# Optimization experiments

Hardware: AMD Instinct MI355X
Metric: run time of the kernel (lower is better)

Reference implementation:

```python
import jax, jax.numpy as jnp
import numpy as np

N_NODES = 500000
N_EDGES = 16000000
NDIM = 2
HID = 8


def setup_inputs() -> dict:
    key = jax.random.key(0)
    ks = jax.random.split(key, 12)
    x = jax.random.normal(ks[0], (N_NODES, NDIM), dtype=jnp.float32)
    edge_index = jax.random.randint(ks[1], (2, N_EDGES), 0, N_NODES, dtype=jnp.int64)
    def lin(k, fan_in, fan_out):
        s = 1.0 / np.sqrt(fan_in)
        return jax.random.uniform(k, (fan_in, fan_out), jnp.float32, -s, s)
    return {
        "x": x,
        "edge_index": edge_index,
        "W1": lin(ks[2], NDIM, HID), "b1": jnp.zeros((HID,), jnp.float32),
        "W2": lin(ks[3], HID, HID), "b2": jnp.zeros((HID,), jnp.float32),
        "W3": lin(ks[4], HID, HID), "b3": jnp.zeros((HID,), jnp.float32),
        "Wr1": lin(ks[5], HID, HID), "br1": jnp.zeros((HID,), jnp.float32),
        "Wr2": lin(ks[6], HID, 1), "br2": jnp.zeros((1,), jnp.float32),
    }


def reference(x, edge_index, W1, b1, W2, b2, W3, b3, Wr1, br1, Wr2, br2):
    N = x.shape[0]
    loop = jnp.arange(N, dtype=edge_index.dtype)
    src = jnp.concatenate([edge_index[0], loop])  # [E+N] message sources j
    dst = jnp.concatenate([edge_index[1], loop])  # [E+N] message targets i
    # GCN symmetric normalization with self-loops: D^{-1/2} (A+I) D^{-1/2}
    deg = jax.ops.segment_sum(jnp.ones(src.shape[0], x.dtype), dst, num_segments=N)
    dinv = jnp.where(deg > 0, jax.lax.rsqrt(jnp.maximum(deg, 1.0)), 0.0)
    norm = (dinv[src] * dinv[dst])[:, None]  # [E+N, 1]

    def gcn_conv(h, W, b):
        h = h @ W  # transform first (small hidden dim)
        agg = jax.ops.segment_sum(h[src] * norm, dst, num_segments=N)
        return agg + b

    h = jax.nn.elu(gcn_conv(x, W1, b1))   # dropout inactive (eval mode)
    h = jax.nn.elu(gcn_conv(h, W2, b2))
    h = jax.nn.elu(gcn_conv(h, W3, b3))
    pooled = jnp.mean(h, axis=0, keepdims=True)  # global_mean_pool, single graph -> [1, HID]
    value = jax.nn.elu(pooled @ Wr1 + br1) @ Wr2 + br2  # [1, 1]
    return value
```

## Files before the change

### kernel.cpp

```cpp
#include <hip/hip_runtime.h>
#include <hip/hip_fp16.h>

#define NNODES 500000
#define HID 8
#define BIN_SHIFT 9
#define BINW 512
#define NBIN 977
#define SCAN_BLK 1024
#define SGRID 256
#define CAP 28
#define BATCH 4096
#define BUFCAP 18432
#define AGRID 512
#define ABLK 256

typedef int intx4 __attribute__((ext_vector_type(4)));

__device__ __forceinline__ unsigned int packh2(float a, float b) {
    __half2 h = __floats2half2_rn(a, b);
    return *reinterpret_cast<unsigned int*>(&h);
}
__device__ __forceinline__ float2 unpackh2(unsigned int u) {
    __half2 h = *reinterpret_cast<__half2*>(&u);
    return __half22float2(h);
}
__device__ __forceinline__ float elu(float t) { return t > 0.0f ? t : expm1f(t); }
__device__ __forceinline__ int nt_load_i(const int* p) { return __builtin_nontemporal_load(p); }
__device__ __forceinline__ intx4 nt_load_i4(const intx4* p) { return __builtin_nontemporal_load(p); }

__device__ __forceinline__ unsigned int enc_e4m3(float x) {
    unsigned sgn = (__float_as_uint(x) >> 31) << 7;
    float ax = fabsf(x);
    if (ax >= 448.f) return sgn | 0x7E;
    if (ax < 0.015625f) {
        unsigned q = (unsigned)__float2int_rn(ax * 512.0f);
        return sgn | q;
    }
    unsigned u = __float_as_uint(ax);
    int te = (int)((u >> 23) & 0xFF) - 120;
    unsigned m = u & 0x7FFFFF;
    unsigned r = (m + 0x7FFFF + ((m >> 20) & 1)) >> 20;
    unsigned code = ((unsigned)te << 3) + r;
    if (code > 0x7E) code = 0x7E;
    return sgn | code;
}

__device__ __forceinline__ float2 dec2_e4m3(unsigned int b01) {
    unsigned int x = (b01 & 0xFFu) | ((b01 & 0xFF00u) << 8);
    unsigned int h = ((x & 0x00800080u) << 8) | ((x & 0x007F007Fu) << 7);
    __half2 hv = *reinterpret_cast<__half2*>(&h);
    const __half2 s256 = __floats2half2_rn(256.0f, 256.0f);
    hv = __hmul2(hv, s256);
    return __half22float2(hv);
}

__global__ void binhist_kernel(const int* __restrict__ dst, int E, int* __restrict__ gbinhist) {
    __shared__ int hist[NBIN];
    for (int b = threadIdx.x; b < NBIN; b += blockDim.x) hist[b] = 0;
    __syncthreads();
    int stride = gridDim.x * blockDim.x;
    const intx4* d4 = (const intx4*)dst;
    int n4 = E >> 2;
    for (int e = blockIdx.x * blockDim.x + threadIdx.x; e < n4; e += stride) {
        intx4 d = nt_load_i4(&d4[e]);
        atomicAdd(&hist[d.x >> BIN_SHIFT], 1);
        atomicAdd(&hist[d.y >> BIN_SHIFT], 1);
        atomicAdd(&hist[d.z >> BIN_SHIFT], 1);
        atomicAdd(&hist[d.w >> BIN_SHIFT], 1);
    }
    int tail0 = n4 << 2;
    for (int e = tail0 + blockIdx.x * blockDim.x + threadIdx.x; e < E; e += stride)
        atomicAdd(&hist[dst[e] >> BIN_SHIFT], 1);
    __syncthreads();
    for (int b = threadIdx.x; b < NBIN; b += blockDim.x) {
        int c = hist[b];
        if (c) atomicAdd(&gbinhist[b], c);
    }
}

__global__ void scan1_kernel(const int* __restrict__ deg, int* __restrict__ excl,
                             int* __restrict__ bsum, int N) {
    __shared__ int sm[SCAN_BLK];
    int tid = threadIdx.x;
    int gid = blockIdx.x * SCAN_BLK + tid;
    int v = (gid < N) ? deg[gid] : 0;
    int x = v;
    sm[tid] = x;
    __syncthreads();
    for (int off = 1; off < SCAN_BLK; off <<= 1) {
        int t = (tid >= off) ? sm[tid - off] : 0;
        __syncthreads();
        x += t;
        sm[tid] = x;
        __syncthreads();
    }
    if (gid < N) excl[gid] = x - v;
    if (tid == SCAN_BLK - 1) bsum[blockIdx.x] = x;
}

__global__ void scan2_kernel(int* __restrict__ bsum, int nb) {
    __shared__ int sm[SCAN_BLK];
    int tid = threadIdx.x;
    int v = (tid < nb) ? bsum[tid] : 0;
    int x = v;
    sm[tid] = x;
    __syncthreads();
    for (int off = 1; off < SCAN_BLK; off <<= 1) {
        int t = (tid >= off) ? sm[tid - off] : 0;
        __syncthreads();
        x += t;
        sm[tid] = x;
        __syncthreads();
    }
    if (tid < nb) bsum[tid] = x - v;
}

__global__ void scan3b_kernel(const int* __restrict__ binexcl, const int* __restrict__ bsum,
                              int* __restrict__ ptr_bins, int* __restrict__ gcursor, int E) {
    int i = blockIdx.x * blockDim.x + threadIdx.x;
    if (i < NBIN) {
        int p = binexcl[i] + bsum[i / SCAN_BLK];
        ptr_bins[i] = p;
        gcursor[i] = p;
    }
    if (i == 0) ptr_bins[NBIN] = E;
}

__global__ void __launch_bounds__(1024) binscatter_kernel(
        const int* __restrict__ src, const int* __restrict__ dst,
        int E, int* __restrict__ gcursor, int* __restrict__ packed) {
    __shared__ int cnt[NBIN];
    __shared__ int bucket[NBIN][CAP];
    __shared__ int fq_bin[NBIN];
    __shared__ int fq_pos[NBIN];
    __shared__ int fq_n;
    int tid = threadIdx.x;
    int slice = (((E + SGRID - 1) / SGRID) + 3) & ~3;
    int e0 = blockIdx.x * slice;
    int e1 = min(E, e0 + slice);
    if (e0 >= e1) return;
    for (int b = tid; b < NBIN; b += 1024) cnt[b] = 0;
    if (tid == 0) fq_n = 0;
    __syncthreads();
    for (int base = e0; base < e1; base += BATCH) {
        int bend = min(e1, base + BATCH);
        int k = base + tid * 4;
        if (k + 4 <= bend) {
            intx4 d = nt_load_i4((const intx4*)(dst + k));
            intx4 s = nt_load_i4((const intx4*)(src + k));
#pragma unroll
            for (int j = 0; j < 4; ++j) {
                int dd = (j == 0) ? d.x : (j == 1) ? d.y : (j == 2) ? d.z : d.w;
                int ss = (j == 0) ? s.x : (j == 1) ? s.y : (j == 2) ? s.z : s.w;
                int b = dd >> BIN_SHIFT;
                int val = (ss << BIN_SHIFT) | (dd & (BINW - 1));
                int slot = atomicAdd(&cnt[b], 1);
                if (slot < CAP) bucket[b][slot] = val;
                else { int gp = atomicAdd(&gcursor[b], 1); packed[gp] = val; }
            }
        } else {
            for (int kk = k; kk < bend; ++kk) {
                int dd = nt_load_i(&dst[kk]);
                int ss = nt_load_i(&src[kk]);
                int b = dd >> BIN_SHIFT;
                int val = (ss << BIN_SHIFT) | (dd & (BINW - 1));
                int slot = atomicAdd(&cnt[b], 1);
                if (slot < CAP) bucket[b][slot] = val;
                else { int gp = atomicAdd(&gcursor[b], 1); packed[gp] = val; }
            }
        }
        __syncthreads();
        if (tid < NBIN) {
            int c = min(cnt[tid], CAP);
            if (c >= 16) {
                int idx = atomicAdd(&fq_n, 1);
                fq_bin[idx] = tid;
                fq_pos[idx] = atomicAdd(&gcursor[tid], 16);
            }
        }
        __syncthreads();
        int nf = fq_n;
        for (int w = tid; w < nf * 16; w += 1024) {
            int q = w >> 4, j = w & 15;
            packed[fq_pos[q] + j] = bucket[fq_bin[q]][j];
        }
        __syncthreads();
        if (tid < NBIN) {
            int c = min(cnt[tid], CAP);
            if (c >= 16) {
                int rem = c - 16;
                for (int j = 0; j < rem; ++j) bucket[tid][j] = bucket[tid][16 + j];
                cnt[tid] = rem;
            } else {
                cnt[tid] = c;
            }
        }
        if (tid == 0) fq_n = 0;
        __syncthreads();
    }
    if (tid < NBIN) {
        int c = min(cnt[tid], CAP);
        if (c > 0) {
            int pos = atomicAdd(&gcursor[tid], c);
            for (int j = 0; j < c; ++j) packed[pos + j] = bucket[tid][j];
        }
    }
}

__global__ void __launch_bounds__(512) binsort_kernel(
        const int* __restrict__ ptr_bins, int* __restrict__ ssrc,
        int* __restrict__ ptr, const float* __restrict__ x,
        unsigned int* __restrict__ t1, int N, int E) {
    __shared__ int buf[BUFCAP];
    __shared__ int hist[BINW];
    __shared__ int scn[BINW];
    __shared__ int cursor[BINW];
    int bin = blockIdx.x;
    int tid = threadIdx.x;
    int base = ptr_bins[bin];
    int len = min(ptr_bins[bin + 1] - base, BUFCAP);
    int node_base = bin << BIN_SHIFT;
    int nn = min(BINW, N - node_base);
    hist[tid] = 0;
    __syncthreads();
    for (int k = tid; k < len; k += 512) {
        int v = nt_load_i(&ssrc[base + k]);
        buf[k] = v;
        atomicAdd(&hist[v & (BINW - 1)], 1);
    }
    __syncthreads();
    int orig = hist[tid];
    int x_ = orig;
    scn[tid] = x_;
    __syncthreads();
    for (int off = 1; off < BINW; off <<= 1) {
        int t = (tid >= off) ? scn[tid - off] : 0;
        __syncthreads();
        x_ += t;
        scn[tid] = x_;
        __syncthreads();
    }
    if (tid < nn) {
        int ex = x_ - orig;
        int node = node_base + tid;
        ptr[node] = base + ex;
        cursor[tid] = ex;
        float dv = rsqrtf((float)orig + 1.0f);
        float2 xv = *reinterpret_cast<const float2*>(x + 2 * (size_t)node);
        t1[node] = packh2(dv * xv.x, dv * xv.y);
    }
    if (bin == NBIN - 1 && tid == 0) ptr[N] = E;
    __syncthreads();
    for (int k = tid; k < len; k += 512) {
        int v = buf[k];
        int pos = atomicAdd(&cursor[v & (BINW - 1)], 1);
        ssrc[base + pos] = v >> BIN_SHIFT;
    }
}

__global__ void __launch_bounds__(ABLK) agg1_kernel(
        const unsigned int* __restrict__ t1, const int* __restrict__ ptr,
        const int* __restrict__ ssrc, const float* __restrict__ W1,
        const float* __restrict__ b1, const float* __restrict__ W2,
        uint2* __restrict__ t2, int N) {
    int stride = AGRID * ABLK;
    for (int i = blockIdx.x * ABLK + threadIdx.x; i < N; i += stride) {
        float2 s = unpackh2(t1[i]);
        int e0 = ptr[i], e1 = ptr[i + 1];
#pragma unroll 8
        for (int k = e0; k < e1; ++k) {
            float2 p = unpackh2(t1[nt_load_i(&ssrc[k])]);
            s.x += p.x; s.y += p.y;
        }
        float dv = rsqrtf((float)(e1 - e0) + 1.0f);
        float h[HID];
#pragma unroll
        for (int c = 0; c < HID; ++c)
            h[c] = elu(dv * (s.x * W1[c] + s.y * W1[HID + c]) + b1[c]);
        float g[HID];
#pragma unroll
        for (int c = 0; c < HID; ++c) {
            float acc = 0.0f;
#pragma unroll
            for (int k = 0; k < HID; ++k) acc += h[k] * W2[k * HID + c];
            g[c] = dv * acc;
        }
        unsigned int lo = enc_e4m3(g[0]) | (enc_e4m3(g[1]) << 8) |
                          (enc_e4m3(g[2]) << 16) | (enc_e4m3(g[3]) << 24);
        unsigned int hi = enc_e4m3(g[4]) | (enc_e4m3(g[5]) << 8) |
                          (enc_e4m3(g[6]) << 16) | (enc_e4m3(g[7]) << 24);
        __builtin_nontemporal_store(lo, &t2[i].x);
        __builtin_nontemporal_store(hi, &t2[i].y);
    }
}

__global__ void __launch_bounds__(ABLK) agg2_kernel(
        const uint2* __restrict__ tab, const int* __restrict__ ptr,
        const int* __restrict__ ssrc, const float* __restrict__ b2,
        const float* __restrict__ W3, uint2* __restrict__ t3, int N) {
    int stride = AGRID * ABLK;
    for (int i = blockIdx.x * ABLK + threadIdx.x; i < N; i += stride) {
        uint2 u = tab[i];
        float2 p0 = dec2_e4m3(u.x), p1 = dec2_e4m3(u.x >> 16);
        float2 p2 = dec2_e4m3(u.y), p3 = dec2_e4m3(u.y >> 16);
        float s0 = p0.x, s1 = p0.y, s2 = p1.x, s3 = p1.y;
        float s4 = p2.x, s5 = p2.y, s6 = p3.x, s7 = p3.y;
        int e0 = ptr[i], e1 = ptr[i + 1];
#pragma unroll 8
        for (int k = e0; k < e1; ++k) {
            uint2 w = tab[nt_load_i(&ssrc[k])];
            float2 q0 = dec2_e4m3(w.x), q1 = dec2_e4m3(w.x >> 16);
            float2 q2 = dec2_e4m3(w.y), q3 = dec2_e4m3(w.y >> 16);
            s0 += q0.x; s1 += q0.y; s2 += q1.x; s3 += q1.y;
            s4 += q2.x; s5 += q2.y; s6 += q3.x; s7 += q3.y;
        }
        float dv = rsqrtf((float)(e1 - e0) + 1.0f);
        float h[HID] = {elu(dv * s0 + b2[0]), elu(dv * s1 + b2[1]),
                        elu(dv * s2 + b2[2]), elu(dv * s3 + b2[3]),
                        elu(dv * s4 + b2[4]), elu(dv * s5 + b2[5]),
                        elu(dv * s6 + b2[6]), elu(dv * s7 + b2[7])};
        float g[HID];
#pragma unroll
        for (int c = 0; c < HID; ++c) {
            float acc = 0.0f;
#pragma unroll
            for (int k = 0; k < HID; ++k) acc += h[k] * W3[k * HID + c];
            g[c] = dv * acc;
        }
        unsigned int lo = enc_e4m3(g[0]) | (enc_e4m3(g[1]) << 8) |
                          (enc_e4m3(g[2]) << 16) | (enc_e4m3(g[3]) << 24);
        unsigned int hi = enc_e4m3(g[4]) | (enc_e4m3(g[5]) << 8) |
                          (enc_e4m3(g[6]) << 16) | (enc_e4m3(g[7]) << 24);
        __builtin_nontemporal_store(lo, &t3[i].x);
        __builtin_nontemporal_store(hi, &t3[i].y);
    }
}

__global__ void __launch_bounds__(ABLK) agg3_kernel(
        const uint2* __restrict__ tab, const int* __restrict__ ptr,
        const int* __restrict__ ssrc, const float* __restrict__ b3,
        double* __restrict__ pooled, int N) {
    float v[HID];
#pragma unroll
    for (int c = 0; c < HID; ++c) v[c] = 0.0f;
    int stride = AGRID * ABLK;
    for (int i = blockIdx.x * ABLK + threadIdx.x; i < N; i += stride) {
        uint2 u = tab[i];
        float2 p0 = dec2_e4m3(u.x), p1 = dec2_e4m3(u.x >> 16);
        float2 p2 = dec2_e4m3(u.y), p3 = dec2_e4m3(u.y >> 16);
        float s0 = p0.x, s1 = p0.y, s2 = p1.x, s3 = p1.y;
        float s4 = p2.x, s5 = p2.y, s6 = p3.x, s7 = p3.y;
        int e0 = ptr[i], e1 = ptr[i + 1];
#pragma unroll 8
        for (int k = e0; k < e1; ++k) {
            uint2 w = tab[nt_load_i(&ssrc[k])];
            float2 q0 = dec2_e4m3(w.x), q1 = dec2_e4m3(w.x >> 16);
            float2 q2 = dec2_e4m3(w.y), q3 = dec2_e4m3(w.y >> 16);
            s0 += q0.x; s1 += q0.y; s2 += q1.x; s3 += q1.y;
            s4 += q2.x; s5 += q2.y; s6 += q3.x; s7 += q3.y;
        }
        float dv = rsqrtf((float)(e1 - e0) + 1.0f);
        v[0] += elu(dv * s0 + b3[0]); v[1] += elu(dv * s1 + b3[1]);
        v[2] += elu(dv * s2 + b3[2]); v[3] += elu(dv * s3 + b3[3]);
        v[4] += elu(dv * s4 + b3[4]); v[5] += elu(dv * s5 + b3[5]);
        v[6] += elu(dv * s6 + b3[6]); v[7] += elu(dv * s7 + b3[7]);
    }
#pragma unroll
    for (int c = 0; c < HID; ++c) {
        float s = v[c];
        for (int off = 32; off > 0; off >>= 1) s += __shfl_down(s, off);
        v[c] = s;
    }
    __shared__ float sm[4][HID];
    int lane = threadIdx.x & 63;
    int wv = threadIdx.x >> 6;
    if (lane == 0) {
#pragma unroll
        for (int c = 0; c < HID; ++c) sm[wv][c] = v[c];
    }
    __syncthreads();
    if (threadIdx.x == 0) {
#pragma unroll
        for (int c = 0; c < HID; ++c) {
            float s = sm[0][c] + sm[1][c] + sm[2][c] + sm[3][c];
            atomicAdd(&pooled[c], (double)s);
        }
    }
}

__global__ void head_kernel(const double* __restrict__ pooled, const float* __restrict__ Wr1,
                            const float* __restrict__ br1, const float* __restrict__ Wr2,
                            const float* __restrict__ br2, float* __restrict__ out, int N) {
    if (threadIdx.x != 0 || blockIdx.x != 0) return;
    float p[HID];
#pragma unroll
    for (int k = 0; k < HID; ++k) p[k] = (float)(pooled[k] / (double)N);
    float hdn[HID];
#pragma unroll
    for (int j = 0; j < HID; ++j) {
        float s = br1[j];
#pragma unroll
        for (int k = 0; k < HID; ++k) s += p[k] * Wr1[k * HID + j];
        hdn[j] = elu(s);
    }
    float v = br2[0];
#pragma unroll
    for (int j = 0; j < HID; ++j) v += hdn[j] * Wr2[j];
    out[0] = v;
}

extern "C" void kernel_launch(void* const* d_in, const int* in_sizes, int n_in,
                              void* d_out, int out_size, void* d_ws, size_t ws_size,
                              hipStream_t stream) {
    const float* x   = (const float*)d_in[0];
    const int*   ei  = (const int*)d_in[1];
    const float* W1  = (const float*)d_in[2];
    const float* b1  = (const float*)d_in[3];
    const float* W2  = (const float*)d_in[4];
    const float* b2  = (const float*)d_in[5];
    const float* W3  = (const float*)d_in[6];
    const float* b3  = (const float*)d_in[7];
    const float* Wr1 = (const float*)d_in[8];
    const float* br1 = (const float*)d_in[9];
    const float* Wr2 = (const float*)d_in[10];
    const float* br2 = (const float*)d_in[11];
    float* out = (float*)d_out;

    const int N = NNODES;
    const int E = in_sizes[1] / 2;
    const int* srcp = ei;
    const int* dstp = ei + E;

    double* pooled    = (double*)d_ws;
    unsigned int* t1  = (unsigned int*)(pooled + HID);
    uint2* t2         = (uint2*)(t1 + N);
    uint2* t3         = t2 + N;
    int* gbinhist     = (int*)(t3 + N);
    int* binexcl      = gbinhist + NBIN;
    int* bsum         = binexcl + NBIN;
    int* ptr_bins     = bsum + 1024;
    int* gcursor      = ptr_bins + NBIN + 1;
    int* ptr          = gcursor + NBIN;
    int* ssrc         = ptr + N + 1;

    hipMemsetAsync(gbinhist, 0, NBIN * sizeof(int), stream);
    hipMemsetAsync(pooled, 0, HID * sizeof(double), stream);

    const int BLK = 256;

    binhist_kernel<<<128, 1024, 0, stream>>>(dstp, E, gbinhist);
    scan1_kernel<<<1, SCAN_BLK, 0, stream>>>(gbinhist, binexcl, bsum, NBIN);
    scan2_kernel<<<1, SCAN_BLK, 0, stream>>>(bsum, 1);
    scan3b_kernel<<<(NBIN + BLK - 1) / BLK, BLK, 0, stream>>>(binexcl, bsum, ptr_bins, gcursor, E);
    binscatter_kernel<<<SGRID, 1024, 0, stream>>>(srcp, dstp, E, gcursor, ssrc);
    binsort_kernel<<<NBIN, 512, 0, stream>>>(ptr_bins, ssrc, ptr, x, t1, N, E);

    agg1_kernel<<<AGRID, ABLK, 0, stream>>>(t1, ptr, ssrc, W1, b1, W2, t2, N);
    agg2_kernel<<<AGRID, ABLK, 0, stream>>>(t2, ptr, ssrc, b2, W3, t3, N);
    agg3_kernel<<<AGRID, ABLK, 0, stream>>>(t3, ptr, ssrc, b3, pooled, N);

    head_kernel<<<1, 64, 0, stream>>>(pooled, Wr1, br1, Wr2, br2, out, N);
}
```

Before: 712.7 us.

## Use edge-balanced per-block aggregation with LDS-staged indices and shared atomics

Each of the three aggregation kernels now handles a 256-node tile per block. The block stages the tile's CSR pointers and up to 9216 source indices into LDS, then splits the tile's edges evenly across threads. A thread finds its first node by binary search and flushes its partial sums into shared-memory accumulators with atomics whenever it crosses a node boundary. This targets load imbalance from per-node degree variance (avg degree ~32) and gives coalesced index loads. In exchange it adds LDS atomics, extra barriers, and fewer gather loads in flight per thread, since each thread walks about 128 edges serially without unrolling.

```diff
diff --git a/kernel.cpp b/kernel.cpp
--- a/kernel.cpp
+++ b/kernel.cpp
@@ -11,8 +11,8 @@
 #define CAP 28
 #define BATCH 4096
 #define BUFCAP 18432
-#define AGRID 512
-#define ABLK 256
+#define ABIN 256
+#define EBUF 9216
 
 typedef int intx4 __attribute__((ext_vector_type(4)));
 
@@ -258,25 +258,56 @@
     }
 }
 
-__global__ void __launch_bounds__(ABLK) agg1_kernel(
+
+__global__ void __launch_bounds__(256) agg1_kernel(
         const unsigned int* __restrict__ t1, const int* __restrict__ ptr,
         const int* __restrict__ ssrc, const float* __restrict__ W1,
         const float* __restrict__ b1, const float* __restrict__ W2,
         uint2* __restrict__ t2, int N) {
-    int stride = AGRID * ABLK;
-    for (int i = blockIdx.x * ABLK + threadIdx.x; i < N; i += stride) {
-        float2 s = unpackh2(t1[i]);
-        int e0 = ptr[i], e1 = ptr[i + 1];
-#pragma unroll 8
-        for (int k = e0; k < e1; ++k) {
-            float2 p = unpackh2(t1[nt_load_i(&ssrc[k])]);
-            s.x += p.x; s.y += p.y;
-        }
-        float dv = rsqrtf((float)(e1 - e0) + 1.0f);
+    __shared__ int lbuf[EBUF];
+    __shared__ int lptr[ABIN + 1];
+    __shared__ float accum[ABIN][2];
+    int tid = threadIdx.x;
+    int n0 = blockIdx.x * ABIN;
+    int nn = min(ABIN, N - n0);
+    for (int j = tid; j <= nn; j += 256) lptr[j] = ptr[n0 + j];
+    if (tid < nn) { accum[tid][0] = 0.f; accum[tid][1] = 0.f; }
+    __syncthreads();
+    int E0 = lptr[0];
+    int len = lptr[nn] - E0;
+    for (int k = tid; k < min(len, EBUF); k += 256) lbuf[k] = nt_load_i(&ssrc[E0 + k]);
+    __syncthreads();
+    int C = (len + ABIN - 1) >> 8;
+    int kb = tid * C, ke = min(len, kb + C);
+    if (kb < ke) {
+        int lo = 0, hi = nn - 1, target = E0 + kb;
+        while (lo < hi) { int mid = (lo + hi + 1) >> 1; if (lptr[mid] <= target) lo = mid; else hi = mid - 1; }
+        int node = lo;
+        float sx = 0.f, sy = 0.f;
+        for (int k = kb; k < ke; ++k) {
+            int eg = E0 + k;
+            if (eg >= lptr[node + 1]) {
+                atomicAdd(&accum[node][0], sx); atomicAdd(&accum[node][1], sy);
+                sx = 0.f; sy = 0.f;
+                do { node++; } while (eg >= lptr[node + 1]);
+            }
+            int sidx = (k < EBUF) ? lbuf[k] : nt_load_i(&ssrc[E0 + k]);
+            float2 p = unpackh2(t1[sidx]);
+            sx += p.x; sy += p.y;
+        }
+        atomicAdd(&accum[node][0], sx); atomicAdd(&accum[node][1], sy);
+    }
+    __syncthreads();
+    if (tid < nn) {
+        int i = n0 + tid;
+        int deg = lptr[tid + 1] - lptr[tid];
+        float dv = rsqrtf((float)deg + 1.0f);
+        float2 sl = unpackh2(t1[i]);
+        float sx = accum[tid][0] + sl.x, sy = accum[tid][1] + sl.y;
         float h[HID];
 #pragma unroll
         for (int c = 0; c < HID; ++c)
-            h[c] = elu(dv * (s.x * W1[c] + s.y * W1[HID + c]) + b1[c]);
+            h[c] = elu(dv * (sx * W1[c] + sy * W1[HID + c]) + b1[c]);
         float g[HID];
 #pragma unroll
         for (int c = 0; c < HID; ++c) {
@@ -294,31 +325,72 @@
     }
 }
 
-__global__ void __launch_bounds__(ABLK) agg2_kernel(
+__global__ void __launch_bounds__(256) agg2_kernel(
         const uint2* __restrict__ tab, const int* __restrict__ ptr,
         const int* __restrict__ ssrc, const float* __restrict__ b2,
         const float* __restrict__ W3, uint2* __restrict__ t3, int N) {
-    int stride = AGRID * ABLK;
-    for (int i = blockIdx.x * ABLK + threadIdx.x; i < N; i += stride) {
-        uint2 u = tab[i];
-        float2 p0 = dec2_e4m3(u.x), p1 = dec2_e4m3(u.x >> 16);
-        float2 p2 = dec2_e4m3(u.y), p3 = dec2_e4m3(u.y >> 16);
-        float s0 = p0.x, s1 = p0.y, s2 = p1.x, s3 = p1.y;
-        float s4 = p2.x, s5 = p2.y, s6 = p3.x, s7 = p3.y;
-        int e0 = ptr[i], e1 = ptr[i + 1];
-#pragma unroll 8
-        for (int k = e0; k < e1; ++k) {
-            uint2 w = tab[nt_load_i(&ssrc[k])];
+    __shared__ int lbuf[EBUF];
+    __shared__ int lptr[ABIN + 1];
+    __shared__ float accum[ABIN][HID];
+    int tid = threadIdx.x;
+    int n0 = blockIdx.x * ABIN;
+    int nn = min(ABIN, N - n0);
+    for (int j = tid; j <= nn; j += 256) lptr[j] = ptr[n0 + j];
+    if (tid < nn) {
+#pragma unroll
+        for (int c = 0; c < HID; ++c) accum[tid][c] = 0.f;
+    }
+    __syncthreads();
+    int E0 = lptr[0];
+    int len = lptr[nn] - E0;
+    for (int k = tid; k < min(len, EBUF); k += 256) lbuf[k] = nt_load_i(&ssrc[E0 + k]);
+    __syncthreads();
+    int C = (len + ABIN - 1) >> 8;
+    int kb = tid * C, ke = min(len, kb + C);
+    if (kb < ke) {
+        int lo = 0, hi = nn - 1, target = E0 + kb;
+        while (lo < hi) { int mid = (lo + hi + 1) >> 1; if (lptr[mid] <= target) lo = mid; else hi = mid - 1; }
+        int node = lo;
+        float s0 = 0.f, s1 = 0.f, s2 = 0.f, s3 = 0.f, s4 = 0.f, s5 = 0.f, s6 = 0.f, s7 = 0.f;
+        for (int k = kb; k < ke; ++k) {
+            int eg = E0 + k;
+            if (eg >= lptr[node + 1]) {
+                atomicAdd(&accum[node][0], s0); atomicAdd(&accum[node][1], s1);
+                atomicAdd(&accum[node][2], s2); atomicAdd(&accum[node][3], s3);
+                atomicAdd(&accum[node][4], s4); atomicAdd(&accum[node][5], s5);
+                atomicAdd(&accum[node][6], s6); atomicAdd(&accum[node][7], s7);
+                s0 = s1 = s2 = s3 = s4 = s5 = s6 = s7 = 0.f;
+                do { node++; } while (eg >= lptr[node + 1]);
+            }
+            int sidx = (k < EBUF) ? lbuf[k] : nt_load_i(&ssrc[E0 + k]);
+            uint2 w = tab[sidx];
             float2 q0 = dec2_e4m3(w.x), q1 = dec2_e4m3(w.x >> 16);
             float2 q2 = dec2_e4m3(w.y), q3 = dec2_e4m3(w.y >> 16);
             s0 += q0.x; s1 += q0.y; s2 += q1.x; s3 += q1.y;
             s4 += q2.x; s5 += q2.y; s6 += q3.x; s7 += q3.y;
         }
-        float dv = rsqrtf((float)(e1 - e0) + 1.0f);
-        float h[HID] = {elu(dv * s0 + b2[0]), elu(dv * s1 + b2[1]),
-                        elu(dv * s2 + b2[2]), elu(dv * s3 + b2[3]),
-                        elu(dv * s4 + b2[4]), elu(dv * s5 + b2[5]),
-                        elu(dv * s6 + b2[6]), elu(dv * s7 + b2[7])};
+        atomicAdd(&accum[node][0], s0); atomicAdd(&accum[node][1], s1);
+        atomicAdd(&accum[node][2], s2); atomicAdd(&accum[node][3], s3);
+        atomicAdd(&accum[node][4], s4); atomicAdd(&accum[node][5], s5);
+        atomicAdd(&accum[node][6], s6); atomicAdd(&accum[node][7], s7);
+    }
+    __syncthreads();
+    if (tid < nn) {
+        int i = n0 + tid;
+        int deg = lptr[tid + 1] - lptr[tid];
+        float dv = rsqrtf((float)deg + 1.0f);
+        uint2 u = tab[i];
+        float2 p0 = dec2_e4m3(u.x), p1 = dec2_e4m3(u.x >> 16);
+        float2 p2 = dec2_e4m3(u.y), p3 = dec2_e4m3(u.y >> 16);
+        float h[HID];
+        h[0] = elu(dv * (accum[tid][0] + p0.x) + b2[0]);
+        h[1] = elu(dv * (accum[tid][1] + p0.y) + b2[1]);
+        h[2] = elu(dv * (accum[tid][2] + p1.x) + b2[2]);
+        h[3] = elu(dv * (accum[tid][3] + p1.y) + b2[3]);
+        h[4] = elu(dv * (accum[tid][4] + p2.x) + b2[4]);
+        h[5] = elu(dv * (accum[tid][5] + p2.y) + b2[5]);
+        h[6] = elu(dv * (accum[tid][6] + p3.x) + b2[6]);
+        h[7] = elu(dv * (accum[tid][7] + p3.y) + b2[7]);
         float g[HID];
 #pragma unroll
         for (int c = 0; c < HID; ++c) {
@@ -336,34 +408,75 @@
     }
 }
 
-__global__ void __launch_bounds__(ABLK) agg3_kernel(
+__global__ void __launch_bounds__(256) agg3_kernel(
         const uint2* __restrict__ tab, const int* __restrict__ ptr,
         const int* __restrict__ ssrc, const float* __restrict__ b3,
         double* __restrict__ pooled, int N) {
-    float v[HID];
-#pragma unroll
-    for (int c = 0; c < HID; ++c) v[c] = 0.0f;
-    int stride = AGRID * ABLK;
-    for (int i = blockIdx.x * ABLK + threadIdx.x; i < N; i += stride) {
-        uint2 u = tab[i];
-        float2 p0 = dec2_e4m3(u.x), p1 = dec2_e4m3(u.x >> 16);
-        float2 p2 = dec2_e4m3(u.y), p3 = dec2_e4m3(u.y >> 16);
-        float s0 = p0.x, s1 = p0.y, s2 = p1.x, s3 = p1.y;
-        float s4 = p2.x, s5 = p2.y, s6 = p3.x, s7 = p3.y;
-        int e0 = ptr[i], e1 = ptr[i + 1];
-#pragma unroll 8
-        for (int k = e0; k < e1; ++k) {
-            uint2 w = tab[nt_load_i(&ssrc[k])];
+    __shared__ int lbuf[EBUF];
+    __shared__ int lptr[ABIN + 1];
+    __shared__ float accum[ABIN][HID];
+    __shared__ float sm[4][HID];
+    int tid = threadIdx.x;
+    int n0 = blockIdx.x * ABIN;
+    int nn = min(ABIN, N - n0);
+    for (int j = tid; j <= nn; j += 256) lptr[j] = ptr[n0 + j];
+    if (tid < nn) {
+#pragma unroll
+        for (int c = 0; c < HID; ++c) accum[tid][c] = 0.f;
+    }
+    __syncthreads();
+    int E0 = lptr[0];
+    int len = lptr[nn] - E0;
+    for (int k = tid; k < min(len, EBUF); k += 256) lbuf[k] = nt_load_i(&ssrc[E0 + k]);
+    __syncthreads();
+    int C = (len + ABIN - 1) >> 8;
+    int kb = tid * C, ke = min(len, kb + C);
+    if (kb < ke) {
+        int lo = 0, hi = nn - 1, target = E0 + kb;
+        while (lo < hi) { int mid = (lo + hi + 1) >> 1; if (lptr[mid] <= target) lo = mid; else hi = mid - 1; }
+        int node = lo;
+        float s0 = 0.f, s1 = 0.f, s2 = 0.f, s3 = 0.f, s4 = 0.f, s5 = 0.f, s6 = 0.f, s7 = 0.f;
+        for (int k = kb; k < ke; ++k) {
+            int eg = E0 + k;
+            if (eg >= lptr[node + 1]) {
+                atomicAdd(&accum[node][0], s0); atomicAdd(&accum[node][1], s1);
+                atomicAdd(&accum[node][2], s2); atomicAdd(&accum[node][3], s3);
+                atomicAdd(&accum[node][4], s4); atomicAdd(&accum[node][5], s5);
+                atomicAdd(&accum[node][6], s6); atomicAdd(&accum[node][7], s7);
+                s0 = s1 = s2 = s3 = s4 = s5 = s6 = s7 = 0.f;
+                do { node++; } while (eg >= lptr[node + 1]);
+            }
+            int sidx = (k < EBUF) ? lbuf[k] : nt_load_i(&ssrc[E0 + k]);
+            uint2 w = tab[sidx];
             float2 q0 = dec2_e4m3(w.x), q1 = dec2_e4m3(w.x >> 16);
             float2 q2 = dec2_e4m3(w.y), q3 = dec2_e4m3(w.y >> 16);
             s0 += q0.x; s1 += q0.y; s2 += q1.x; s3 += q1.y;
             s4 += q2.x; s5 += q2.y; s6 += q3.x; s7 += q3.y;
         }
-        float dv = rsqrtf((float)(e1 - e0) + 1.0f);
-        v[0] += elu(dv * s0 + b3[0]); v[1] += elu(dv * s1 + b3[1]);
-        v[2] += elu(dv * s2 + b3[2]); v[3] += elu(dv * s3 + b3[3]);
-        v[4] += elu(dv * s4 + b3[4]); v[5] += elu(dv * s5 + b3[5]);
-        v[6] += elu(dv * s6 + b3[6]); v[7] += elu(dv * s7 + b3[7]);
+        atomicAdd(&accum[node][0], s0); atomicAdd(&accum[node][1], s1);
+        atomicAdd(&accum[node][2], s2); atomicAdd(&accum[node][3], s3);
+        atomicAdd(&accum[node][4], s4); atomicAdd(&accum[node][5], s5);
+        atomicAdd(&accum[node][6], s6); atomicAdd(&accum[node][7], s7);
+    }
+    __syncthreads();
+    float v[HID];
+#pragma unroll
+    for (int c = 0; c < HID; ++c) v[c] = 0.f;
+    if (tid < nn) {
+        int i = n0 + tid;
+        int deg = lptr[tid + 1] - lptr[tid];
+        float dv = rsqrtf((float)deg + 1.0f);
+        uint2 u = tab[i];
+        float2 p0 = dec2_e4m3(u.x), p1 = dec2_e4m3(u.x >> 16);
+        float2 p2 = dec2_e4m3(u.y), p3 = dec2_e4m3(u.y >> 16);
+        v[0] = elu(dv * (accum[tid][0] + p0.x) + b3[0]);
+        v[1] = elu(dv * (accum[tid][1] + p0.y) + b3[1]);
+        v[2] = elu(dv * (accum[tid][2] + p1.x) + b3[2]);
+        v[3] = elu(dv * (accum[tid][3] + p1.y) + b3[3]);
+        v[4] = elu(dv * (accum[tid][4] + p2.x) + b3[4]);
+        v[5] = elu(dv * (accum[tid][5] + p2.y) + b3[5]);
+        v[6] = elu(dv * (accum[tid][6] + p3.x) + b3[6]);
+        v[7] = elu(dv * (accum[tid][7] + p3.y) + b3[7]);
     }
 #pragma unroll
     for (int c = 0; c < HID; ++c) {
@@ -371,7 +484,6 @@
         for (int off = 32; off > 0; off >>= 1) s += __shfl_down(s, off);
         v[c] = s;
     }
-    __shared__ float sm[4][HID];
     int lane = threadIdx.x & 63;
     int wv = threadIdx.x >> 6;
     if (lane == 0) {
@@ -447,6 +559,7 @@
     hipMemsetAsync(pooled, 0, HID * sizeof(double), stream);
 
     const int BLK = 256;
+    const int aggGrid = (N + ABIN - 1) / ABIN;
 
     binhist_kernel<<<128, 1024, 0, stream>>>(dstp, E, gbinhist);
     scan1_kernel<<<1, SCAN_BLK, 0, stream>>>(gbinhist, binexcl, bsum, NBIN);
@@ -455,9 +568,9 @@
     binscatter_kernel<<<SGRID, 1024, 0, stream>>>(srcp, dstp, E, gcursor, ssrc);
     binsort_kernel<<<NBIN, 512, 0, stream>>>(ptr_bins, ssrc, ptr, x, t1, N, E);
 
-    agg1_kernel<<<AGRID, ABLK, 0, stream>>>(t1, ptr, ssrc, W1, b1, W2, t2, N);
-    agg2_kernel<<<AGRID, ABLK, 0, stream>>>(t2, ptr, ssrc, b2, W3, t3, N);
-    agg3_kernel<<<AGRID, ABLK, 0, stream>>>(t3, ptr, ssrc, b3, pooled, N);
+    agg1_kernel<<<aggGrid, BLK, 0, stream>>>(t1, ptr, ssrc, W1, b1, W2, t2, N);
+    agg2_kernel<<<aggGrid, BLK, 0, stream>>>(t2, ptr, ssrc, b2, W3, t3, N);
+    agg3_kernel<<<aggGrid, BLK, 0, stream>>>(t3, ptr, ssrc, b3, pooled, N);
 
     head_kernel<<<1, 64, 0, stream>>>(pooled, Wr1, br1, Wr2, br2, out, N);
 }
```

Measured after the change: 772.3 us. 8.4% more time.

## Stage per-block CSR neighbor indices in LDS with coalesced loads

Applied to the files above, without the earlier changes.

The aggregation kernels switch from a grid-stride loop to one block per 256 destination nodes. Each block first loads its contiguous ssrc segment into shared memory with coalesced loads, using an XOR swizzle against bank conflicts. Threads then read neighbor indices from LDS instead of making strided per-thread global loads. Segments longer than the buffer fall back to global loads. The cost is about 37KB of LDS per block, which limits occupancy, plus two block barriers, and agg3 now issues one atomic per block across many more blocks (~1954).

```diff
diff --git a/kernel.cpp b/kernel.cpp
--- a/kernel.cpp
+++ b/kernel.cpp
@@ -11,8 +11,9 @@
 #define CAP 28
 #define BATCH 4096
 #define BUFCAP 18432
-#define AGRID 512
-#define ABLK 256
+#define ABIN 256
+#define EBUF 9216
+#define LIDX(k) ((k) ^ (((k) >> 5) & 31))
 
 typedef int intx4 __attribute__((ext_vector_type(4)));
 
@@ -258,112 +259,150 @@
     }
 }
 
-__global__ void __launch_bounds__(ABLK) agg1_kernel(
+__global__ void __launch_bounds__(256) agg1_kernel(
         const unsigned int* __restrict__ t1, const int* __restrict__ ptr,
         const int* __restrict__ ssrc, const float* __restrict__ W1,
         const float* __restrict__ b1, const float* __restrict__ W2,
         uint2* __restrict__ t2, int N) {
-    int stride = AGRID * ABLK;
-    for (int i = blockIdx.x * ABLK + threadIdx.x; i < N; i += stride) {
-        float2 s = unpackh2(t1[i]);
-        int e0 = ptr[i], e1 = ptr[i + 1];
+    __shared__ int lbuf[EBUF];
+    __shared__ int lptr[ABIN + 1];
+    int tid = threadIdx.x;
+    int n0 = blockIdx.x * ABIN;
+    int nn = min(ABIN, N - n0);
+    for (int j = tid; j <= nn; j += 256) lptr[j] = ptr[n0 + j];
+    __syncthreads();
+    int E0 = lptr[0];
+    int len = lptr[nn] - E0;
+    int lim = min(len, EBUF);
+    for (int k = tid; k < lim; k += 256) lbuf[LIDX(k)] = nt_load_i(&ssrc[E0 + k]);
+    __syncthreads();
+    if (tid >= nn) return;
+    int i = n0 + tid;
+    int kb = lptr[tid] - E0, ke = lptr[tid + 1] - E0;
+    float2 s = unpackh2(t1[i]);
 #pragma unroll 8
-        for (int k = e0; k < e1; ++k) {
-            float2 p = unpackh2(t1[nt_load_i(&ssrc[k])]);
-            s.x += p.x; s.y += p.y;
-        }
-        float dv = rsqrtf((float)(e1 - e0) + 1.0f);
-        float h[HID];
-#pragma unroll
-        for (int c = 0; c < HID; ++c)
-            h[c] = elu(dv * (s.x * W1[c] + s.y * W1[HID + c]) + b1[c]);
-        float g[HID];
-#pragma unroll
-        for (int c = 0; c < HID; ++c) {
-            float acc = 0.0f;
-#pragma unroll
-            for (int k = 0; k < HID; ++k) acc += h[k] * W2[k * HID + c];
-            g[c] = dv * acc;
-        }
-        unsigned int lo = enc_e4m3(g[0]) | (enc_e4m3(g[1]) << 8) |
-                          (enc_e4m3(g[2]) << 16) | (enc_e4m3(g[3]) << 24);
-        unsigned int hi = enc_e4m3(g[4]) | (enc_e4m3(g[5]) << 8) |
-                          (enc_e4m3(g[6]) << 16) | (enc_e4m3(g[7]) << 24);
-        __builtin_nontemporal_store(lo, &t2[i].x);
-        __builtin_nontemporal_store(hi, &t2[i].y);
-    }
-}
-
-__global__ void __launch_bounds__(ABLK) agg2_kernel(
+    for (int k = kb; k < ke; ++k) {
+        int sidx = (k < EBUF) ? lbuf[LIDX(k)] : nt_load_i(&ssrc[E0 + k]);
+        float2 p = unpackh2(t1[sidx]);
+        s.x += p.x; s.y += p.y;
+    }
+    float dv = rsqrtf((float)(ke - kb) + 1.0f);
+    float h[HID];
+#pragma unroll
+    for (int c = 0; c < HID; ++c)
+        h[c] = elu(dv * (s.x * W1[c] + s.y * W1[HID + c]) + b1[c]);
+    float g[HID];
+#pragma unroll
+    for (int c = 0; c < HID; ++c) {
+        float acc = 0.0f;
+#pragma unroll
+        for (int k = 0; k < HID; ++k) acc += h[k] * W2[k * HID + c];
+        g[c] = dv * acc;
+    }
+    unsigned int lo = enc_e4m3(g[0]) | (enc_e4m3(g[1]) << 8) |
+                      (enc_e4m3(g[2]) << 16) | (enc_e4m3(g[3]) << 24);
+    unsigned int hi = enc_e4m3(g[4]) | (enc_e4m3(g[5]) << 8) |
+                      (enc_e4m3(g[6]) << 16) | (enc_e4m3(g[7]) << 24);
+    __builtin_nontemporal_store(lo, &t2[i].x);
+    __builtin_nontemporal_store(hi, &t2[i].y);
+}
+
+__global__ void __launch_bounds__(256) agg2_kernel(
         const uint2* __restrict__ tab, const int* __restrict__ ptr,
         const int* __restrict__ ssrc, const float* __restrict__ b2,
         const float* __restrict__ W3, uint2* __restrict__ t3, int N) {
-    int stride = AGRID * ABLK;
-    for (int i = blockIdx.x * ABLK + threadIdx.x; i < N; i += stride) {
+    __shared__ int lbuf[EBUF];
+    __shared__ int lptr[ABIN + 1];
+    int tid = threadIdx.x;
+    int n0 = blockIdx.x * ABIN;
+    int nn = min(ABIN, N - n0);
+    for (int j = tid; j <= nn; j += 256) lptr[j] = ptr[n0 + j];
+    __syncthreads();
+    int E0 = lptr[0];
+    int len = lptr[nn] - E0;
+    int lim = min(len, EBUF);
+    for (int k = tid; k < lim; k += 256) lbuf[LIDX(k)] = nt_load_i(&ssrc[E0 + k]);
+    __syncthreads();
+    if (tid >= nn) return;
+    int i = n0 + tid;
+    int kb = lptr[tid] - E0, ke = lptr[tid + 1] - E0;
+    uint2 u = tab[i];
+    float2 p0 = dec2_e4m3(u.x), p1 = dec2_e4m3(u.x >> 16);
+    float2 p2 = dec2_e4m3(u.y), p3 = dec2_e4m3(u.y >> 16);
+    float s0 = p0.x, s1 = p0.y, s2 = p1.x, s3 = p1.y;
+    float s4 = p2.x, s5 = p2.y, s6 = p3.x, s7 = p3.y;
+#pragma unroll 8
+    for (int k = kb; k < ke; ++k) {
+        int sidx = (k < EBUF) ? lbuf[LIDX(k)] : nt_load_i(&ssrc[E0 + k]);
+        uint2 w = tab[sidx];
+        float2 q0 = dec2_e4m3(w.x), q1 = dec2_e4m3(w.x >> 16);
+        float2 q2 = dec2_e4m3(w.y), q3 = dec2_e4m3(w.y >> 16);
+        s0 += q0.x; s1 += q0.y; s2 += q1.x; s3 += q1.y;
+        s4 += q2.x; s5 += q2.y; s6 += q3.x; s7 += q3.y;
+    }
+    float dv = rsqrtf((float)(ke - kb) + 1.0f);
+    float h[HID] = {elu(dv * s0 + b2[0]), elu(dv * s1 + b2[1]),
+                    elu(dv * s2 + b2[2]), elu(dv * s3 + b2[3]),
+                    elu(dv * s4 + b2[4]), elu(dv * s5 + b2[5]),
+                    elu(dv * s6 + b2[6]), elu(dv * s7 + b2[7])};
+    float g[HID];
+#pragma unroll
+    for (int c = 0; c < HID; ++c) {
+        float acc = 0.0f;
+#pragma unroll
+        for (int k = 0; k < HID; ++k) acc += h[k] * W3[k * HID + c];
+        g[c] = dv * acc;
+    }
+    unsigned int lo = enc_e4m3(g[0]) | (enc_e4m3(g[1]) << 8) |
+                      (enc_e4m3(g[2]) << 16) | (enc_e4m3(g[3]) << 24);
+    unsigned int hi = enc_e4m3(g[4]) | (enc_e4m3(g[5]) << 8) |
+                      (enc_e4m3(g[6]) << 16) | (enc_e4m3(g[7]) << 24);
+    __builtin_nontemporal_store(lo, &t3[i].x);
+    __builtin_nontemporal_store(hi, &t3[i].y);
+}
+
+__global__ void __launch_bounds__(256) agg3_kernel(
+        const uint2* __restrict__ tab, const int* __restrict__ ptr,
+        const int* __restrict__ ssrc, const float* __restrict__ b3,
+        double* __restrict__ pooled, int N) {
+    __shared__ int lbuf[EBUF];
+    __shared__ int lptr[ABIN + 1];
+    __shared__ float sm[4][HID];
+    int tid = threadIdx.x;
+    int n0 = blockIdx.x * ABIN;
+    int nn = min(ABIN, N - n0);
+    for (int j = tid; j <= nn; j += 256) lptr[j] = ptr[n0 + j];
+    __syncthreads();
+    int E0 = lptr[0];
+    int len = lptr[nn] - E0;
+    int lim = min(len, EBUF);
+    for (int k = tid; k < lim; k += 256) lbuf[LIDX(k)] = nt_load_i(&ssrc[E0 + k]);
+    __syncthreads();
+    float v[HID];
+#pragma unroll
+    for (int c = 0; c < HID; ++c) v[c] = 0.f;
+    if (tid < nn) {
+        int i = n0 + tid;
+        int kb = lptr[tid] - E0, ke = lptr[tid + 1] - E0;
         uint2 u = tab[i];
         float2 p0 = dec2_e4m3(u.x), p1 = dec2_e4m3(u.x >> 16);
         float2 p2 = dec2_e4m3(u.y), p3 = dec2_e4m3(u.y >> 16);
         float s0 = p0.x, s1 = p0.y, s2 = p1.x, s3 = p1.y;
         float s4 = p2.x, s5 = p2.y, s6 = p3.x, s7 = p3.y;
-        int e0 = ptr[i], e1 = ptr[i + 1];
 #pragma unroll 8
-        for (int k = e0; k < e1; ++k) {
-            uint2 w = tab[nt_load_i(&ssrc[k])];
+        for (int k = kb; k < ke; ++k) {
+            int sidx = (k < EBUF) ? lbuf[LIDX(k)] : nt_load_i(&ssrc[E0 + k]);
+            uint2 w = tab[sidx];
             float2 q0 = dec2_e4m3(w.x), q1 = dec2_e4m3(w.x >> 16);
             float2 q2 = dec2_e4m3(w.y), q3 = dec2_e4m3(w.y >> 16);
             s0 += q0.x; s1 += q0.y; s2 += q1.x; s3 += q1.y;
             s4 += q2.x; s5 += q2.y; s6 += q3.x; s7 += q3.y;
         }
-        float dv = rsqrtf((float)(e1 - e0) + 1.0f);
-        float h[HID] = {elu(dv * s0 + b2[0]), elu(dv * s1 + b2[1]),
-                        elu(dv * s2 + b2[2]), elu(dv * s3 + b2[3]),
-                        elu(dv * s4 + b2[4]), elu(dv * s5 + b2[5]),
-                        elu(dv * s6 + b2[6]), elu(dv * s7 + b2[7])};
-        float g[HID];
-#pragma unroll
-        for (int c = 0; c < HID; ++c) {
-            float acc = 0.0f;
-#pragma unroll
-            for (int k = 0; k < HID; ++k) acc += h[k] * W3[k * HID + c];
-            g[c] = dv * acc;
-        }
-        unsigned int lo = enc_e4m3(g[0]) | (enc_e4m3(g[1]) << 8) |
-                          (enc_e4m3(g[2]) << 16) | (enc_e4m3(g[3]) << 24);
-        unsigned int hi = enc_e4m3(g[4]) | (enc_e4m3(g[5]) << 8) |
-                          (enc_e4m3(g[6]) << 16) | (enc_e4m3(g[7]) << 24);
-        __builtin_nontemporal_store(lo, &t3[i].x);
-        __builtin_nontemporal_store(hi, &t3[i].y);
-    }
-}
-
-__global__ void __launch_bounds__(ABLK) agg3_kernel(
-        const uint2* __restrict__ tab, const int* __restrict__ ptr,
-        const int* __restrict__ ssrc, const float* __restrict__ b3,
-        double* __restrict__ pooled, int N) {
-    float v[HID];
-#pragma unroll
-    for (int c = 0; c < HID; ++c) v[c] = 0.0f;
-    int stride = AGRID * ABLK;
-    for (int i = blockIdx.x * ABLK + threadIdx.x; i < N; i += stride) {
-        uint2 u = tab[i];
-        float2 p0 = dec2_e4m3(u.x), p1 = dec2_e4m3(u.x >> 16);
-        float2 p2 = dec2_e4m3(u.y), p3 = dec2_e4m3(u.y >> 16);
-        float s0 = p0.x, s1 = p0.y, s2 = p1.x, s3 = p1.y;
-        float s4 = p2.x, s5 = p2.y, s6 = p3.x, s7 = p3.y;
-        int e0 = ptr[i], e1 = ptr[i + 1];
-#pragma unroll 8
-        for (int k = e0; k < e1; ++k) {
-            uint2 w = tab[nt_load_i(&ssrc[k])];
-            float2 q0 = dec2_e4m3(w.x), q1 = dec2_e4m3(w.x >> 16);
-            float2 q2 = dec2_e4m3(w.y), q3 = dec2_e4m3(w.y >> 16);
-            s0 += q0.x; s1 += q0.y; s2 += q1.x; s3 += q1.y;
-            s4 += q2.x; s5 += q2.y; s6 += q3.x; s7 += q3.y;
-        }
-        float dv = rsqrtf((float)(e1 - e0) + 1.0f);
-        v[0] += elu(dv * s0 + b3[0]); v[1] += elu(dv * s1 + b3[1]);
-        v[2] += elu(dv * s2 + b3[2]); v[3] += elu(dv * s3 + b3[3]);
-        v[4] += elu(dv * s4 + b3[4]); v[5] += elu(dv * s5 + b3[5]);
-        v[6] += elu(dv * s6 + b3[6]); v[7] += elu(dv * s7 + b3[7]);
+        float dv = rsqrtf((float)(ke - kb) + 1.0f);
+        v[0] = elu(dv * s0 + b3[0]); v[1] = elu(dv * s1 + b3[1]);
+        v[2] = elu(dv * s2 + b3[2]); v[3] = elu(dv * s3 + b3[3]);
+        v[4] = elu(dv * s4 + b3[4]); v[5] = elu(dv * s5 + b3[5]);
+        v[6] = elu(dv * s6 + b3[6]); v[7] = elu(dv * s7 + b3[7]);
     }
 #pragma unroll
     for (int c = 0; c < HID; ++c) {
@@ -371,7 +410,6 @@
         for (int off = 32; off > 0; off >>= 1) s += __shfl_down(s, off);
         v[c] = s;
     }
-    __shared__ float sm[4][HID];
     int lane = threadIdx.x & 63;
     int wv = threadIdx.x >> 6;
     if (lane == 0) {
@@ -447,6 +485,7 @@
     hipMemsetAsync(pooled, 0, HID * sizeof(double), stream);
 
     const int BLK = 256;
+    const int aggGrid = (N + ABIN - 1) / ABIN;
 
     binhist_kernel<<<128, 1024, 0, stream>>>(dstp, E, gbinhist);
     scan1_kernel<<<1, SCAN_BLK, 0, stream>>>(gbinhist, binexcl, bsum, NBIN);
@@ -455,9 +494,9 @@
     binscatter_kernel<<<SGRID, 1024, 0, stream>>>(srcp, dstp, E, gcursor, ssrc);
     binsort_kernel<<<NBIN, 512, 0, stream>>>(ptr_bins, ssrc, ptr, x, t1, N, E);
 
-    agg1_kernel<<<AGRID, ABLK, 0, stream>>>(t1, ptr, ssrc, W1, b1, W2, t2, N);
-    agg2_kernel<<<AGRID, ABLK, 0, stream>>>(t2, ptr, ssrc, b2, W3, t3, N);
-    agg3_kernel<<<AGRID, ABLK, 0, stream>>>(t3, ptr, ssrc, b3, pooled, N);
+    agg1_kernel<<<aggGrid, BLK, 0, stream>>>(t1, ptr, ssrc, W1, b1, W2, t2, N);
+    agg2_kernel<<<aggGrid, BLK, 0, stream>>>(t2, ptr, ssrc, b2, W3, t3, N);
+    agg3_kernel<<<aggGrid, BLK, 0, stream>>>(t3, ptr, ssrc, b3, pooled, N);
 
     head_kernel<<<1, 64, 0, stream>>>(pooled, Wr1, br1, Wr2, br2, out, N);
 }
```

Result: no change. 721.3 us (+1.2%).

## Split layer-2/3 gathers into two source-half passes for cache locality

Applied to the files above, without the earlier changes.

Each node's CSR neighbor list is partitioned by whether the source node is in the lower or upper half of the node range, and a mid pointer is recorded. Layers 2 and 3 are each split into two kernels: the first gathers only lower-half sources and writes fp32 partial sums, the second gathers upper-half sources, adds the partials and finishes. The aim is to halve the randomly accessed feature table footprint per pass so it fits better in L2/LLC. In exchange it adds two kernel launches and a 32-byte-per-node partial-sum write and read per layer.

```diff
diff --git a/kernel.cpp b/kernel.cpp
--- a/kernel.cpp
+++ b/kernel.cpp
@@ -209,43 +209,49 @@
 
 __global__ void __launch_bounds__(512) binsort_kernel(
         const int* __restrict__ ptr_bins, int* __restrict__ ssrc,
-        int* __restrict__ ptr, const float* __restrict__ x,
-        unsigned int* __restrict__ t1, int N, int E) {
+        int* __restrict__ ptr, int* __restrict__ mid, const float* __restrict__ x,
+        unsigned int* __restrict__ t1, int N, int E, int halfN) {
     __shared__ int buf[BUFCAP];
-    __shared__ int hist[BINW];
-    __shared__ int scn[BINW];
-    __shared__ int cursor[BINW];
+    __shared__ int hist2[2 * BINW];
+    __shared__ int scnP[BINW];
+    __shared__ int cursor[2 * BINW];
     int bin = blockIdx.x;
     int tid = threadIdx.x;
     int base = ptr_bins[bin];
     int len = min(ptr_bins[bin + 1] - base, BUFCAP);
     int node_base = bin << BIN_SHIFT;
     int nn = min(BINW, N - node_base);
-    hist[tid] = 0;
+    hist2[tid] = 0;
+    hist2[tid + BINW] = 0;
     __syncthreads();
     for (int k = tid; k < len; k += 512) {
         int v = nt_load_i(&ssrc[base + k]);
         buf[k] = v;
-        atomicAdd(&hist[v & (BINW - 1)], 1);
-    }
-    __syncthreads();
-    int orig = hist[tid];
-    int x_ = orig;
-    scn[tid] = x_;
+        int key = ((v & (BINW - 1)) << 1) | ((v >> BIN_SHIFT) >= halfN ? 1 : 0);
+        atomicAdd(&hist2[key], 1);
+    }
+    __syncthreads();
+    int cA = hist2[2 * tid], cB = hist2[2 * tid + 1];
+    int pairsum = cA + cB;
+    int xs = pairsum;
+    scnP[tid] = xs;
     __syncthreads();
     for (int off = 1; off < BINW; off <<= 1) {
-        int t = (tid >= off) ? scn[tid - off] : 0;
-        __syncthreads();
-        x_ += t;
-        scn[tid] = x_;
-        __syncthreads();
-    }
+        int t = (tid >= off) ? scnP[tid - off] : 0;
+        __syncthreads();
+        xs += t;
+        scnP[tid] = xs;
+        __syncthreads();
+    }
+    int exA = xs - pairsum;
+    int exB = exA + cA;
+    cursor[2 * tid] = exA;
+    cursor[2 * tid + 1] = exB;
     if (tid < nn) {
-        int ex = x_ - orig;
         int node = node_base + tid;
-        ptr[node] = base + ex;
-        cursor[tid] = ex;
-        float dv = rsqrtf((float)orig + 1.0f);
+        ptr[node] = base + exA;
+        mid[node] = base + exB;
+        float dv = rsqrtf((float)pairsum + 1.0f);
         float2 xv = *reinterpret_cast<const float2*>(x + 2 * (size_t)node);
         t1[node] = packh2(dv * xv.x, dv * xv.y);
     }
@@ -253,7 +259,8 @@
     __syncthreads();
     for (int k = tid; k < len; k += 512) {
         int v = buf[k];
-        int pos = atomicAdd(&cursor[v & (BINW - 1)], 1);
+        int key = ((v & (BINW - 1)) << 1) | ((v >> BIN_SHIFT) >= halfN ? 1 : 0);
+        int pos = atomicAdd(&cursor[key], 1);
         ssrc[base + pos] = v >> BIN_SHIFT;
     }
 }
@@ -282,7 +289,7 @@
         for (int c = 0; c < HID; ++c) {
             float acc = 0.0f;
 #pragma unroll
-            for (int k = 0; k < HID; ++k) acc += h[k] * W2[k * HID + c];
+            for (int k2 = 0; k2 < HID; ++k2) acc += h[k2] * W2[k2 * HID + c];
             g[c] = dv * acc;
         }
         unsigned int lo = enc_e4m3(g[0]) | (enc_e4m3(g[1]) << 8) |
@@ -294,27 +301,67 @@
     }
 }
 
-__global__ void __launch_bounds__(ABLK) agg2_kernel(
+#define GATHER8(sidx)                                                         \
+    {                                                                         \
+        uint2 w = tab[sidx];                                                  \
+        float2 q0 = dec2_e4m3(w.x), q1 = dec2_e4m3(w.x >> 16);                \
+        float2 q2 = dec2_e4m3(w.y), q3 = dec2_e4m3(w.y >> 16);                \
+        s0 += q0.x; s1 += q0.y; s2 += q1.x; s3 += q1.y;                       \
+        s4 += q2.x; s5 += q2.y; s6 += q3.x; s7 += q3.y;                       \
+    }
+
+__global__ void __launch_bounds__(ABLK) aggA_kernel(
         const uint2* __restrict__ tab, const int* __restrict__ ptr,
-        const int* __restrict__ ssrc, const float* __restrict__ b2,
-        const float* __restrict__ W3, uint2* __restrict__ t3, int N) {
+        const int* __restrict__ mid, const int* __restrict__ ssrc,
+        float4* __restrict__ part, int N, int halfN) {
     int stride = AGRID * ABLK;
     for (int i = blockIdx.x * ABLK + threadIdx.x; i < N; i += stride) {
-        uint2 u = tab[i];
-        float2 p0 = dec2_e4m3(u.x), p1 = dec2_e4m3(u.x >> 16);
-        float2 p2 = dec2_e4m3(u.y), p3 = dec2_e4m3(u.y >> 16);
-        float s0 = p0.x, s1 = p0.y, s2 = p1.x, s3 = p1.y;
-        float s4 = p2.x, s5 = p2.y, s6 = p3.x, s7 = p3.y;
-        int e0 = ptr[i], e1 = ptr[i + 1];
-#pragma unroll 8
-        for (int k = e0; k < e1; ++k) {
-            uint2 w = tab[nt_load_i(&ssrc[k])];
+        float s0 = 0.f, s1 = 0.f, s2 = 0.f, s3 = 0.f, s4 = 0.f, s5 = 0.f, s6 = 0.f, s7 = 0.f;
+        if (i < halfN) {
+            uint2 w = tab[i];
             float2 q0 = dec2_e4m3(w.x), q1 = dec2_e4m3(w.x >> 16);
             float2 q2 = dec2_e4m3(w.y), q3 = dec2_e4m3(w.y >> 16);
             s0 += q0.x; s1 += q0.y; s2 += q1.x; s3 += q1.y;
             s4 += q2.x; s5 += q2.y; s6 += q3.x; s7 += q3.y;
         }
-        float dv = rsqrtf((float)(e1 - e0) + 1.0f);
+        int e0 = ptr[i], e1 = mid[i];
+#pragma unroll 8
+        for (int k = e0; k < e1; ++k) GATHER8(nt_load_i(&ssrc[k]));
+        float4 lo4 = make_float4(s0, s1, s2, s3);
+        float4 hi4 = make_float4(s4, s5, s6, s7);
+        __builtin_nontemporal_store(lo4.x, &part[2 * (size_t)i].x);
+        __builtin_nontemporal_store(lo4.y, &part[2 * (size_t)i].y);
+        __builtin_nontemporal_store(lo4.z, &part[2 * (size_t)i].z);
+        __builtin_nontemporal_store(lo4.w, &part[2 * (size_t)i].w);
+        __builtin_nontemporal_store(hi4.x, &part[2 * (size_t)i + 1].x);
+        __builtin_nontemporal_store(hi4.y, &part[2 * (size_t)i + 1].y);
+        __builtin_nontemporal_store(hi4.z, &part[2 * (size_t)i + 1].z);
+        __builtin_nontemporal_store(hi4.w, &part[2 * (size_t)i + 1].w);
+    }
+}
+
+__global__ void __launch_bounds__(ABLK) agg2B_kernel(
+        const uint2* __restrict__ tab, const int* __restrict__ ptr,
+        const int* __restrict__ mid, const int* __restrict__ ssrc,
+        const float4* __restrict__ part, const float* __restrict__ b2,
+        const float* __restrict__ W3, uint2* __restrict__ t3, int N, int halfN) {
+    int stride = AGRID * ABLK;
+    for (int i = blockIdx.x * ABLK + threadIdx.x; i < N; i += stride) {
+        float4 lo4 = part[2 * (size_t)i], hi4 = part[2 * (size_t)i + 1];
+        float s0 = lo4.x, s1 = lo4.y, s2 = lo4.z, s3 = lo4.w;
+        float s4 = hi4.x, s5 = hi4.y, s6 = hi4.z, s7 = hi4.w;
+        if (i >= halfN) {
+            uint2 w = tab[i];
+            float2 q0 = dec2_e4m3(w.x), q1 = dec2_e4m3(w.x >> 16);
+            float2 q2 = dec2_e4m3(w.y), q3 = dec2_e4m3(w.y >> 16);
+            s0 += q0.x; s1 += q0.y; s2 += q1.x; s3 += q1.y;
+            s4 += q2.x; s5 += q2.y; s6 += q3.x; s7 += q3.y;
+        }
+        int e0 = mid[i], e1 = ptr[i + 1];
+#pragma unroll 8
+        for (int k = e0; k < e1; ++k) GATHER8(nt_load_i(&ssrc[k]));
+        int deg = e1 - ptr[i];
+        float dv = rsqrtf((float)deg + 1.0f);
         float h[HID] = {elu(dv * s0 + b2[0]), elu(dv * s1 + b2[1]),
                         elu(dv * s2 + b2[2]), elu(dv * s3 + b2[3]),
                         elu(dv * s4 + b2[4]), elu(dv * s5 + b2[5]),
@@ -324,7 +371,7 @@
         for (int c = 0; c < HID; ++c) {
             float acc = 0.0f;
 #pragma unroll
-            for (int k = 0; k < HID; ++k) acc += h[k] * W3[k * HID + c];
+            for (int k2 = 0; k2 < HID; ++k2) acc += h[k2] * W3[k2 * HID + c];
             g[c] = dv * acc;
         }
         unsigned int lo = enc_e4m3(g[0]) | (enc_e4m3(g[1]) << 8) |
@@ -336,30 +383,31 @@
     }
 }
 
-__global__ void __launch_bounds__(ABLK) agg3_kernel(
+__global__ void __launch_bounds__(ABLK) agg3B_kernel(
         const uint2* __restrict__ tab, const int* __restrict__ ptr,
-        const int* __restrict__ ssrc, const float* __restrict__ b3,
-        double* __restrict__ pooled, int N) {
+        const int* __restrict__ mid, const int* __restrict__ ssrc,
+        const float4* __restrict__ part, const float* __restrict__ b3,
+        double* __restrict__ pooled, int N, int halfN) {
     float v[HID];
 #pragma unroll
     for (int c = 0; c < HID; ++c) v[c] = 0.0f;
     int stride = AGRID * ABLK;
     for (int i = blockIdx.x * ABLK + threadIdx.x; i < N; i += stride) {
-        uint2 u = tab[i];
-        float2 p0 = dec2_e4m3(u.x), p1 = dec2_e4m3(u.x >> 16);
-        float2 p2 = dec2_e4m3(u.y), p3 = dec2_e4m3(u.y >> 16);
-        float s0 = p0.x, s1 = p0.y, s2 = p1.x, s3 = p1.y;
-        float s4 = p2.x, s5 = p2.y, s6 = p3.x, s7 = p3.y;
-        int e0 = ptr[i], e1 = ptr[i + 1];
-#pragma unroll 8
-        for (int k = e0; k < e1; ++k) {
-            uint2 w = tab[nt_load_i(&ssrc[k])];
+        float4 lo4 = part[2 * (size_t)i], hi4 = part[2 * (size_t)i + 1];
+        float s0 = lo4.x, s1 = lo4.y, s2 = lo4.z, s3 = lo4.w;
+        float s4 = hi4.x, s5 = hi4.y, s6 = hi4.z, s7 = hi4.w;
+        if (i >= halfN) {
+            uint2 w = tab[i];
             float2 q0 = dec2_e4m3(w.x), q1 = dec2_e4m3(w.x >> 16);
             float2 q2 = dec2_e4m3(w.y), q3 = dec2_e4m3(w.y >> 16);
             s0 += q0.x; s1 += q0.y; s2 += q1.x; s3 += q1.y;
             s4 += q2.x; s5 += q2.y; s6 += q3.x; s7 += q3.y;
         }
-        float dv = rsqrtf((float)(e1 - e0) + 1.0f);
+        int e0 = mid[i], e1 = ptr[i + 1];
+#pragma unroll 8
+        for (int k = e0; k < e1; ++k) GATHER8(nt_load_i(&ssrc[k]));
+        int deg = e1 - ptr[i];
+        float dv = rsqrtf((float)deg + 1.0f);
         v[0] += elu(dv * s0 + b3[0]); v[1] += elu(dv * s1 + b3[1]);
         v[2] += elu(dv * s2 + b3[2]); v[3] += elu(dv * s3 + b3[3]);
         v[4] += elu(dv * s4 + b3[4]); v[5] += elu(dv * s5 + b3[5]);
@@ -427,12 +475,14 @@
     float* out = (float*)d_out;
 
     const int N = NNODES;
+    const int halfN = N / 2;
     const int E = in_sizes[1] / 2;
     const int* srcp = ei;
     const int* dstp = ei + E;
 
     double* pooled    = (double*)d_ws;
-    unsigned int* t1  = (unsigned int*)(pooled + HID);
+    float4* part      = (float4*)(pooled + HID);
+    unsigned int* t1  = (unsigned int*)(part + 2 * (size_t)N);
     uint2* t2         = (uint2*)(t1 + N);
     uint2* t3         = t2 + N;
     int* gbinhist     = (int*)(t3 + N);
@@ -441,7 +491,8 @@
     int* ptr_bins     = bsum + 1024;
     int* gcursor      = ptr_bins + NBIN + 1;
     int* ptr          = gcursor + NBIN;
-    int* ssrc         = ptr + N + 1;
+    int* mid          = ptr + N + 1;
+    int* ssrc         = mid + N;
 
     hipMemsetAsync(gbinhist, 0, NBIN * sizeof(int), stream);
     hipMemsetAsync(pooled, 0, HID * sizeof(double), stream);
@@ -453,11 +504,13 @@
     scan2_kernel<<<1, SCAN_BLK, 0, stream>>>(bsum, 1);
     scan3b_kernel<<<(NBIN + BLK - 1) / BLK, BLK, 0, stream>>>(binexcl, bsum, ptr_bins, gcursor, E);
     binscatter_kernel<<<SGRID, 1024, 0, stream>>>(srcp, dstp, E, gcursor, ssrc);
-    binsort_kernel<<<NBIN, 512, 0, stream>>>(ptr_bins, ssrc, ptr, x, t1, N, E);
+    binsort_kernel<<<NBIN, 512, 0, stream>>>(ptr_bins, ssrc, ptr, mid, x, t1, N, E, halfN);
 
     agg1_kernel<<<AGRID, ABLK, 0, stream>>>(t1, ptr, ssrc, W1, b1, W2, t2, N);
-    agg2_kernel<<<AGRID, ABLK, 0, stream>>>(t2, ptr, ssrc, b2, W3, t3, N);
-    agg3_kernel<<<AGRID, ABLK, 0, stream>>>(t3, ptr, ssrc, b3, pooled, N);
+    aggA_kernel<<<AGRID, ABLK, 0, stream>>>(t2, ptr, mid, ssrc, part, N, halfN);
+    agg2B_kernel<<<AGRID, ABLK, 0, stream>>>(t2, ptr, mid, ssrc, part, b2, W3, t3, N, halfN);
+    aggA_kernel<<<AGRID, ABLK, 0, stream>>>(t3, ptr, mid, ssrc, part, N, halfN);
+    agg3B_kernel<<<AGRID, ABLK, 0, stream>>>(t3, ptr, mid, ssrc, part, b3, pooled, N, halfN);
 
     head_kernel<<<1, 64, 0, stream>>>(pooled, Wr1, br1, Wr2, br2, out, N);
 }
```

Measured after the change: 836.1 us. 1.17x slower.
